# Performance work log

Hardware: AMD Instinct MI355X
Metric: run time of the kernel (lower is better)

Reference implementation:

```python
import jax, jax.numpy as jnp
import numpy as np

B, S = 8, 512          # batch, seq_len
D, F = 1024, 2048      # d_model, head hidden dim
H = 16                 # num_tasks (= num heads)
V = 3000               # selfies vocab
O = 1                  # head output size
INIT = 0.02


def setup_inputs() -> dict:
    key = jax.random.key(0)
    ks = jax.random.split(key, 12)
    return {
        "selfies": jax.random.randint(ks[0], (B, S), 0, V),
        "tasks": jax.random.randint(ks[1], (B, S), 0, H + 1),  # 0 -> invalid (-1)
        "values": jax.random.normal(ks[2], (B, S), jnp.float32),
        "property_mask": jax.random.randint(ks[3], (B, S), 0, 2).astype(bool),
        # shared_base params (embed + FFN -> [B,S,D])
        "emb_selfies": jax.random.normal(ks[4], (V, D), jnp.float32) * INIT,
        "emb_tasks": jax.random.normal(ks[5], (H + 1, D), jnp.float32) * INIT,
        "val_vec": jax.random.normal(ks[6], (D,), jnp.float32) * INIT,
        "Ws": jax.random.normal(ks[7], (D, D), jnp.float32) * INIT,
        "bs": jnp.zeros((D,), jnp.float32),
        # stacked per-head MLP params: Linear(D,F) -> GELU -> Linear(F,O)
        "W1": jax.random.normal(ks[8], (H, D, F), jnp.float32) * INIT,
        "b1": jnp.zeros((H, F), jnp.float32),
        "W2": jax.random.normal(ks[9], (H, F, O), jnp.float32) * INIT,
        "b2": jnp.zeros((H, O), jnp.float32),
    }


def reference(selfies, tasks, values, property_mask,
              emb_selfies, emb_tasks, val_vec, Ws, bs, W1, b1, W2, b2):
    # ---- shared_base: embed + masked token features + FFN -> [B,S,D] ----
    h = (emb_selfies[selfies] + emb_tasks[tasks] + values[..., None] * val_vec)
    h = h * property_mask[..., None].astype(h.dtype)
    shared = jax.nn.gelu(h @ Ws + bs)                      # [B,S,D]

    # ---- routing: task token -> head index, 0 means invalid (-1) ----
    head_idx = jnp.where(tasks > 0, (tasks - 1) % H, -1)   # [B,S]

    # ---- each active head runs its MLP over the FULL shared_output ----
    hid = jax.nn.gelu(jnp.einsum('bsd,hdf->bshf', shared, W1) + b1)  # [B,S,H,F]
    heads_out = jnp.einsum('bshf,hfo->bsho', hid, W2) + b2           # [B,S,H,O]

    # ---- scatter/select per token by head index; invalid -> zeros ----
    idx = jnp.clip(head_idx, 0)
    out = jnp.take_along_axis(heads_out, idx[..., None, None], axis=2)[:, :, 0, :]
    return jnp.where(head_idx[..., None] >= 0, out, jnp.zeros_like(out))
```

## Files before the change

### kernel.cpp

```cpp
#include <hip/hip_runtime.h>
#include <hip/hip_bf16.h>

#define TOK 4096
#define DD  1024
#define FF  2048
#define NH  16

typedef short bf16x8 __attribute__((ext_vector_type(8)));
typedef float f32x4  __attribute__((ext_vector_type(4)));

__device__ __forceinline__ float gelu_f(float x) {
  float u = 0.7978845608028654f * (x + 0.044715f * x * x * x);
  float e = __expf(2.0f * u);
  return 0.5f * x * (2.0f - 2.0f / (e + 1.0f));
}

__device__ __forceinline__ unsigned short f2bf(float f) {
  union { float f; unsigned u; } v; v.f = f;
  unsigned r = v.u + 0x7FFF + ((v.u >> 16) & 1);
  return (unsigned short)(r >> 16);
}
__device__ __forceinline__ unsigned pack2(float a, float b) {
  return (unsigned)f2bf(a) | ((unsigned)f2bf(b) << 16);
}

__device__ __forceinline__ void load_lds16(const void* g, void* l) {
  __builtin_amdgcn_global_load_lds(
      (const __attribute__((address_space(1))) void*)g,
      (__attribute__((address_space(3))) void*)l, 16, 0, 0);
}

__global__ __launch_bounds__(256) void route_kernel(
    const int* __restrict__ tasks, const float* __restrict__ b2,
    int* __restrict__ counts, int* __restrict__ lists, float* __restrict__ out) {
  int t = blockIdx.x * 256 + threadIdx.x;
  if (t >= TOK) return;
  int task = tasks[t];
  if (task > 0) {
    int h = (task - 1) & (NH - 1);
    int pos = atomicAdd(&counts[h], 1);
    lists[h * TOK + pos] = t;
    out[t] = b2[h];
  } else {
    out[t] = 0.0f;
  }
}

__global__ __launch_bounds__(256) void prep_x(
    const int* __restrict__ selfies, const int* __restrict__ tasks,
    const float* __restrict__ values, const int* __restrict__ pmask,
    const float* __restrict__ emb_s, const float* __restrict__ emb_t,
    const float* __restrict__ val_vec, unsigned short* __restrict__ Xb) {
  int gid = blockIdx.x * 256 + threadIdx.x;
  int kc = (gid & 127) * 8;
  int t  = gid >> 7;
  int sid = selfies[t], tsk = tasks[t];
  float v = values[t];
  float msk = pmask[t] ? 1.0f : 0.0f;
  const float* ps = emb_s + (size_t)sid * DD + kc;
  const float* pt = emb_t + (size_t)tsk * DD + kc;
  const float* pv = val_vec + kc;
  float r[8];
#pragma unroll
  for (int j = 0; j < 8; j += 4) {
    float4 a = *(const float4*)(ps + j);
    float4 b = *(const float4*)(pt + j);
    float4 c = *(const float4*)(pv + j);
    r[j + 0] = (a.x + b.x + v * c.x) * msk;
    r[j + 1] = (a.y + b.y + v * c.y) * msk;
    r[j + 2] = (a.z + b.z + v * c.z) * msk;
    r[j + 3] = (a.w + b.w + v * c.w) * msk;
  }
  uint4 o;
  o.x = pack2(r[0], r[1]); o.y = pack2(r[2], r[3]);
  o.z = pack2(r[4], r[5]); o.w = pack2(r[6], r[7]);
  *(uint4*)(Xb + (size_t)gid * 8) = o;
}

__global__ __launch_bounds__(256) void prep_w(
    const float* __restrict__ Ws, const float* __restrict__ W1,
    unsigned short* __restrict__ Wsp, unsigned short* __restrict__ W1p) {
  int cid = blockIdx.x * 256 + threadIdx.x;
  const float* src;
  unsigned short* dst;
  int stride;
  if (cid < 16 * 128 * 32 * 64) {
    int lane = cid & 63, kc2 = (cid >> 6) & 31, nt = (cid >> 11) & 127, h = cid >> 18;
    src = W1 + ((size_t)h * DD + kc2 * 32 + (lane >> 4) * 8) * FF + nt * 16 + (lane & 15);
    dst = W1p + (size_t)cid * 8;
    stride = FF;
  } else {
    int cid2 = cid - 16 * 128 * 32 * 64;
    int lane = cid2 & 63, kc2 = (cid2 >> 6) & 31, nt = cid2 >> 11;
    src = Ws + ((size_t)kc2 * 32 + (lane >> 4) * 8) * DD + nt * 16 + (lane & 15);
    dst = Wsp + (size_t)cid2 * 8;
    stride = DD;
  }
  float r[8];
#pragma unroll
  for (int j = 0; j < 8; ++j) r[j] = src[(size_t)j * stride];
  uint4 o;
  o.x = pack2(r[0], r[1]); o.y = pack2(r[2], r[3]);
  o.z = pack2(r[4], r[5]); o.w = pack2(r[6], r[7]);
  *(uint4*)dst = o;
}

__global__ __launch_bounds__(256) void gemm1_mfma(
    const unsigned short* __restrict__ Xb, const unsigned short* __restrict__ Wsp,
    const float* __restrict__ bs, unsigned short* __restrict__ shared_bf) {
  __shared__ __align__(16) unsigned short As[2 * 4 * 64 * 8];
  __shared__ __align__(16) unsigned short Bs[2 * 8 * 64 * 8];

  const int tid = threadIdx.x;
  const int lane = tid & 63, w = tid >> 6;
  const int m0 = blockIdx.x * 64;
  const int n0 = blockIdx.y * 128;
  const int q = lane >> 4, c = lane & 15;

  const unsigned short* aSrc = Xb + (size_t)(m0 + w * 16 + c) * DD + q * 8;
  unsigned short* aDst0 = As + (size_t)(0 * 256 + w * 64 + lane) * 8;
  unsigned short* aDst1 = As + (size_t)(1 * 256 + w * 64 + lane) * 8;

  const unsigned short* bBase = Wsp + ((size_t)(blockIdx.y * 8 + w * 2)) * 32 * 512 + lane * 8;
  f32x4 acc[4][2] = {};

  for (int k0 = 0; k0 < DD; k0 += 64) {
    load_lds16(aSrc + k0, aDst0);
    load_lds16(aSrc + k0 + 32, aDst1);
    const unsigned short* bk = bBase + k0 * 16;
#pragma unroll
    for (int i = 0; i < 4; ++i) {
      int kk = i >> 1, t = i & 1;
      load_lds16(bk + (size_t)t * 16384 + kk * 512,
                 Bs + (size_t)(kk * 8 + w * 2 + t) * 512 + lane * 8);
    }
    __syncthreads();
#pragma unroll
    for (int kk = 0; kk < 2; ++kk) {
      bf16x8 a[4], b[2];
#pragma unroll
      for (int mt = 0; mt < 4; ++mt)
        a[mt] = *(const bf16x8*)(As + (size_t)((kk * 4 + mt) * 64 + lane) * 8);
#pragma unroll
      for (int t = 0; t < 2; ++t)
        b[t] = *(const bf16x8*)(Bs + (size_t)((kk * 8 + w * 2 + t) * 64 + lane) * 8);
#pragma unroll
      for (int mt = 0; mt < 4; ++mt)
#pragma unroll
        for (int t = 0; t < 2; ++t)
          acc[mt][t] = __builtin_amdgcn_mfma_f32_16x16x32_bf16(a[mt], b[t], acc[mt][t], 0, 0, 0);
    }
    __syncthreads();
  }

  float bsv[2];
#pragma unroll
  for (int t = 0; t < 2; ++t) bsv[t] = bs[n0 + w * 32 + t * 16 + c];
#pragma unroll
  for (int mt = 0; mt < 4; ++mt)
#pragma unroll
    for (int t = 0; t < 2; ++t)
#pragma unroll
      for (int r = 0; r < 4; ++r) {
        int row = m0 + mt * 16 + q * 4 + r;
        int col = n0 + w * 32 + t * 16 + c;
        shared_bf[(size_t)row * DD + col] = f2bf(gelu_f(acc[mt][t][r] + bsv[t]));
      }
}

__global__ __launch_bounds__(256) void gemm2_mfma(
    const unsigned short* __restrict__ shared_bf, const unsigned short* __restrict__ W1p,
    const float* __restrict__ b1, const float* __restrict__ W2,
    const int* __restrict__ counts, const int* __restrict__ lists,
    float* __restrict__ out) {
  const int h = blockIdx.z;
  const int nt_h = counts[h];
  const int m0 = blockIdx.x * 64;
  if (m0 >= nt_h) return;
  const int fc = blockIdx.y;

  __shared__ __align__(16) unsigned short As[2 * 4 * 64 * 8];
  __shared__ __align__(16) unsigned short Bs[2 * 16 * 64 * 8];
  __shared__ int   stok[64];
  __shared__ float red[4][68];

  const int tid = threadIdx.x;
  const int lane = tid & 63, w = tid >> 6;
  const int q = lane >> 4, c = lane & 15;

  if (tid < 64) {
    int i = m0 + tid;
    stok[tid] = (i < nt_h) ? lists[h * TOK + i] : -1;
  }
  __syncthreads();

  int tokr = stok[w * 16 + c];
  if (tokr < 0) tokr = 0;
  const unsigned short* aSrc = shared_bf + (size_t)tokr * DD + q * 8;
  unsigned short* aDst0 = As + (size_t)(0 * 256 + w * 64 + lane) * 8;
  unsigned short* aDst1 = As + (size_t)(1 * 256 + w * 64 + lane) * 8;

  const unsigned short* bBase =
      W1p + ((size_t)h * 128 + fc * 16 + w * 4) * 32 * 512 + lane * 8;

  f32x4 acc[4][4] = {};

  for (int k0 = 0; k0 < DD; k0 += 64) {
    load_lds16(aSrc + k0, aDst0);
    load_lds16(aSrc + k0 + 32, aDst1);
    const unsigned short* bk = bBase + k0 * 16;
#pragma unroll
    for (int i = 0; i < 8; ++i) {
      int kk = i >> 2, t = i & 3;
      load_lds16(bk + (size_t)t * 16384 + kk * 512,
                 Bs + (size_t)(kk * 16 + w * 4 + t) * 512 + lane * 8);
    }
    __syncthreads();
#pragma unroll
    for (int kk = 0; kk < 2; ++kk) {
      bf16x8 a[4], b[4];
#pragma unroll
      for (int mt = 0; mt < 4; ++mt)
        a[mt] = *(const bf16x8*)(As + (size_t)((kk * 4 + mt) * 64 + lane) * 8);
#pragma unroll
      for (int t = 0; t < 4; ++t)
        b[t] = *(const bf16x8*)(Bs + (size_t)((kk * 16 + w * 4 + t) * 64 + lane) * 8);
#pragma unroll
      for (int mt = 0; mt < 4; ++mt)
#pragma unroll
        for (int t = 0; t < 4; ++t)
          acc[mt][t] = __builtin_amdgcn_mfma_f32_16x16x32_bf16(a[mt], b[t], acc[mt][t], 0, 0, 0);
    }
    __syncthreads();
  }

  const float* b1h = b1 + (size_t)h * FF + fc * 256 + w * 64;
  const float* w2h = W2 + (size_t)h * FF + fc * 256 + w * 64;
  float b1v[4], w2v[4];
#pragma unroll
  for (int t = 0; t < 4; ++t) { b1v[t] = b1h[t * 16 + c]; w2v[t] = w2h[t * 16 + c]; }

#pragma unroll
  for (int mt = 0; mt < 4; ++mt)
#pragma unroll
    for (int r = 0; r < 4; ++r) {
      float s = 0.0f;
#pragma unroll
      for (int t = 0; t < 4; ++t)
        s += gelu_f(acc[mt][t][r] + b1v[t]) * w2v[t];
      s += __shfl_xor(s, 1);
      s += __shfl_xor(s, 2);
      s += __shfl_xor(s, 4);
      s += __shfl_xor(s, 8);
      if (c == 0) red[w][mt * 16 + q * 4 + r] = s;
    }
  __syncthreads();

  if (tid < 64) {
    int t = stok[tid];
    if (t >= 0) {
      float s = red[0][tid] + red[1][tid] + red[2][tid] + red[3][tid];
      atomicAdd(&out[t], s);
    }
  }
}

extern "C" void kernel_launch(void* const* d_in, const int* in_sizes, int n_in,
                              void* d_out, int out_size, void* d_ws, size_t ws_size,
                              hipStream_t stream) {
  const int*   selfies = (const int*)d_in[0];
  const int*   tasks   = (const int*)d_in[1];
  const float* values  = (const float*)d_in[2];
  const int*   pmask   = (const int*)d_in[3];
  const float* emb_s   = (const float*)d_in[4];
  const float* emb_t   = (const float*)d_in[5];
  const float* val_vec = (const float*)d_in[6];
  const float* Ws      = (const float*)d_in[7];
  const float* bs      = (const float*)d_in[8];
  const float* W1      = (const float*)d_in[9];
  const float* b1      = (const float*)d_in[10];
  const float* W2      = (const float*)d_in[11];
  const float* b2      = (const float*)d_in[12];
  float* out = (float*)d_out;

  char* ws = (char*)d_ws;
  unsigned short* Xb        = (unsigned short*)ws;
  unsigned short* shared_bf = (unsigned short*)(ws + (8u << 20));
  unsigned short* Wsp       = (unsigned short*)(ws + (16u << 20));
  unsigned short* W1p       = (unsigned short*)(ws + (18u << 20));
  int* counts = (int*)(ws + (82u << 20));
  int* lists  = (int*)(ws + (82u << 20) + 256);

  hipMemsetAsync(counts, 0, NH * sizeof(int), stream);
  route_kernel<<<TOK / 256, 256, 0, stream>>>(tasks, b2, counts, lists, out);
  prep_x<<<TOK * 128 / 256, 256, 0, stream>>>(selfies, tasks, values, pmask,
                                              emb_s, emb_t, val_vec, Xb);
  prep_w<<<(16 * 128 * 32 * 64 + 64 * 32 * 64) / 256, 256, 0, stream>>>(Ws, W1, Wsp, W1p);
  gemm1_mfma<<<dim3(TOK / 64, DD / 128), 256, 0, stream>>>(Xb, Wsp, bs, shared_bf);
  gemm2_mfma<<<dim3(8, FF / 256, NH), 256, 0, stream>>>(shared_bf, W1p, b1, W2,
                                                        counts, lists, out);
}
```

Baseline: 353.0 us.

## Double-buffer LDS in both GEMMs and halve gemm2 N-tile width

Both MFMA GEMM kernels now keep two LDS buffers, so the next k-slice is loaded while the current one is computed, with one barrier per iteration instead of two. gemm2 also narrows its F tile from 256 to 128 columns per block and doubles the grid along F, which lowers accumulator register use and adds more blocks. The cost is reloading the A tile twice as often in gemm2 and using more LDS per block.

Result: no change. 358.8 us (+1.6%).

```diff
diff --git a/kernel.cpp b/kernel.cpp
--- a/kernel.cpp
+++ b/kernel.cpp
@@ -108,8 +108,8 @@
 __global__ __launch_bounds__(256) void gemm1_mfma(
     const unsigned short* __restrict__ Xb, const unsigned short* __restrict__ Wsp,
     const float* __restrict__ bs, unsigned short* __restrict__ shared_bf) {
-  __shared__ __align__(16) unsigned short As[2 * 4 * 64 * 8];
-  __shared__ __align__(16) unsigned short Bs[2 * 8 * 64 * 8];
+  __shared__ __align__(16) unsigned short As[2][2 * 4 * 64 * 8];
+  __shared__ __align__(16) unsigned short Bs[2][2 * 8 * 64 * 8];
 
   const int tid = threadIdx.x;
   const int lane = tid & 63, w = tid >> 6;
@@ -118,40 +118,48 @@
   const int q = lane >> 4, c = lane & 15;
 
   const unsigned short* aSrc = Xb + (size_t)(m0 + w * 16 + c) * DD + q * 8;
-  unsigned short* aDst0 = As + (size_t)(0 * 256 + w * 64 + lane) * 8;
-  unsigned short* aDst1 = As + (size_t)(1 * 256 + w * 64 + lane) * 8;
-
   const unsigned short* bBase = Wsp + ((size_t)(blockIdx.y * 8 + w * 2)) * 32 * 512 + lane * 8;
   f32x4 acc[4][2] = {};
 
-  for (int k0 = 0; k0 < DD; k0 += 64) {
-    load_lds16(aSrc + k0, aDst0);
-    load_lds16(aSrc + k0 + 32, aDst1);
+  auto stage = [&](int buf, int k0) {
+    load_lds16(aSrc + k0,      As[buf] + (size_t)(0 * 256 + w * 64 + lane) * 8);
+    load_lds16(aSrc + k0 + 32, As[buf] + (size_t)(1 * 256 + w * 64 + lane) * 8);
     const unsigned short* bk = bBase + k0 * 16;
 #pragma unroll
     for (int i = 0; i < 4; ++i) {
       int kk = i >> 1, t = i & 1;
       load_lds16(bk + (size_t)t * 16384 + kk * 512,
-                 Bs + (size_t)(kk * 8 + w * 2 + t) * 512 + lane * 8);
-    }
-    __syncthreads();
+                 Bs[buf] + (size_t)(kk * 8 + w * 2 + t) * 512 + lane * 8);
+    }
+  };
+  auto compute = [&](int buf) {
 #pragma unroll
     for (int kk = 0; kk < 2; ++kk) {
       bf16x8 a[4], b[2];
 #pragma unroll
       for (int mt = 0; mt < 4; ++mt)
-        a[mt] = *(const bf16x8*)(As + (size_t)((kk * 4 + mt) * 64 + lane) * 8);
+        a[mt] = *(const bf16x8*)(As[buf] + (size_t)((kk * 4 + mt) * 64 + lane) * 8);
 #pragma unroll
       for (int t = 0; t < 2; ++t)
-        b[t] = *(const bf16x8*)(Bs + (size_t)((kk * 8 + w * 2 + t) * 64 + lane) * 8);
+        b[t] = *(const bf16x8*)(Bs[buf] + (size_t)((kk * 8 + w * 2 + t) * 64 + lane) * 8);
 #pragma unroll
       for (int mt = 0; mt < 4; ++mt)
 #pragma unroll
         for (int t = 0; t < 2; ++t)
           acc[mt][t] = __builtin_amdgcn_mfma_f32_16x16x32_bf16(a[mt], b[t], acc[mt][t], 0, 0, 0);
     }
+  };
+
+  stage(0, 0);
+  __syncthreads();
+  int cur = 0;
+  for (int k0 = 64; k0 < DD; k0 += 64) {
+    stage(cur ^ 1, k0);
+    compute(cur);
     __syncthreads();
-  }
+    cur ^= 1;
+  }
+  compute(cur);
 
   float bsv[2];
 #pragma unroll
@@ -179,8 +187,8 @@
   if (m0 >= nt_h) return;
   const int fc = blockIdx.y;
 
-  __shared__ __align__(16) unsigned short As[2 * 4 * 64 * 8];
-  __shared__ __align__(16) unsigned short Bs[2 * 16 * 64 * 8];
+  __shared__ __align__(16) unsigned short As[2][2 * 4 * 64 * 8];
+  __shared__ __align__(16) unsigned short Bs[2][2 * 8 * 64 * 8];
   __shared__ int   stok[64];
   __shared__ float red[4][68];
 
@@ -197,48 +205,57 @@
   int tokr = stok[w * 16 + c];
   if (tokr < 0) tokr = 0;
   const unsigned short* aSrc = shared_bf + (size_t)tokr * DD + q * 8;
-  unsigned short* aDst0 = As + (size_t)(0 * 256 + w * 64 + lane) * 8;
-  unsigned short* aDst1 = As + (size_t)(1 * 256 + w * 64 + lane) * 8;
 
   const unsigned short* bBase =
-      W1p + ((size_t)h * 128 + fc * 16 + w * 4) * 32 * 512 + lane * 8;
-
-  f32x4 acc[4][4] = {};
-
-  for (int k0 = 0; k0 < DD; k0 += 64) {
-    load_lds16(aSrc + k0, aDst0);
-    load_lds16(aSrc + k0 + 32, aDst1);
+      W1p + ((size_t)h * 128 + fc * 8 + w * 2) * 32 * 512 + lane * 8;
+
+  f32x4 acc[4][2] = {};
+
+  auto stage = [&](int buf, int k0) {
+    load_lds16(aSrc + k0,      As[buf] + (size_t)(0 * 256 + w * 64 + lane) * 8);
+    load_lds16(aSrc + k0 + 32, As[buf] + (size_t)(1 * 256 + w * 64 + lane) * 8);
     const unsigned short* bk = bBase + k0 * 16;
 #pragma unroll
-    for (int i = 0; i < 8; ++i) {
-      int kk = i >> 2, t = i & 3;
+    for (int i = 0; i < 4; ++i) {
+      int kk = i >> 1, t = i & 1;
       load_lds16(bk + (size_t)t * 16384 + kk * 512,
-                 Bs + (size_t)(kk * 16 + w * 4 + t) * 512 + lane * 8);
-    }
+                 Bs[buf] + (size_t)(kk * 8 + w * 2 + t) * 512 + lane * 8);
+    }
+  };
+  auto compute = [&](int buf) {
+#pragma unroll
+    for (int kk = 0; kk < 2; ++kk) {
+      bf16x8 a[4], b[2];
+#pragma unroll
+      for (int mt = 0; mt < 4; ++mt)
+        a[mt] = *(const bf16x8*)(As[buf] + (size_t)((kk * 4 + mt) * 64 + lane) * 8);
+#pragma unroll
+      for (int t = 0; t < 2; ++t)
+        b[t] = *(const bf16x8*)(Bs[buf] + (size_t)((kk * 8 + w * 2 + t) * 64 + lane) * 8);
+#pragma unroll
+      for (int mt = 0; mt < 4; ++mt)
+#pragma unroll
+        for (int t = 0; t < 2; ++t)
+          acc[mt][t] = __builtin_amdgcn_mfma_f32_16x16x32_bf16(a[mt], b[t], acc[mt][t], 0, 0, 0);
+    }
+  };
+
+  stage(0, 0);
+  __syncthreads();
+  int cur = 0;
+  for (int k0 = 64; k0 < DD; k0 += 64) {
+    stage(cur ^ 1, k0);
+    compute(cur);
     __syncthreads();
-#pragma unroll
-    for (int kk = 0; kk < 2; ++kk) {
-      bf16x8 a[4], b[4];
-#pragma unroll
-      for (int mt = 0; mt < 4; ++mt)
-        a[mt] = *(const bf16x8*)(As + (size_t)((kk * 4 + mt) * 64 + lane) * 8);
-#pragma unroll
-      for (int t = 0; t < 4; ++t)
-        b[t] = *(const bf16x8*)(Bs + (size_t)((kk * 16 + w * 4 + t) * 64 + lane) * 8);
-#pragma unroll
-      for (int mt = 0; mt < 4; ++mt)
-#pragma unroll
-        for (int t = 0; t < 4; ++t)
-          acc[mt][t] = __builtin_amdgcn_mfma_f32_16x16x32_bf16(a[mt], b[t], acc[mt][t], 0, 0, 0);
-    }
-    __syncthreads();
-  }
-
-  const float* b1h = b1 + (size_t)h * FF + fc * 256 + w * 64;
-  const float* w2h = W2 + (size_t)h * FF + fc * 256 + w * 64;
-  float b1v[4], w2v[4];
-#pragma unroll
-  for (int t = 0; t < 4; ++t) { b1v[t] = b1h[t * 16 + c]; w2v[t] = w2h[t * 16 + c]; }
+    cur ^= 1;
+  }
+  compute(cur);
+
+  const float* b1h = b1 + (size_t)h * FF + fc * 128 + w * 32;
+  const float* w2h = W2 + (size_t)h * FF + fc * 128 + w * 32;
+  float b1v[2], w2v[2];
+#pragma unroll
+  for (int t = 0; t < 2; ++t) { b1v[t] = b1h[t * 16 + c]; w2v[t] = w2h[t * 16 + c]; }
 
 #pragma unroll
   for (int mt = 0; mt < 4; ++mt)
@@ -246,7 +263,7 @@
     for (int r = 0; r < 4; ++r) {
       float s = 0.0f;
 #pragma unroll
-      for (int t = 0; t < 4; ++t)
+      for (int t = 0; t < 2; ++t)
         s += gelu_f(acc[mt][t][r] + b1v[t]) * w2v[t];
       s += __shfl_xor(s, 1);
       s += __shfl_xor(s, 2);
@@ -297,6 +314,6 @@
                                               emb_s, emb_t, val_vec, Xb);
   prep_w<<<(16 * 128 * 32 * 64 + 64 * 32 * 64) / 256, 256, 0, stream>>>(Ws, W1, Wsp, W1p);
   gemm1_mfma<<<dim3(TOK / 64, DD / 128), 256, 0, stream>>>(Xb, Wsp, bs, shared_bf);
-  gemm2_mfma<<<dim3(8, FF / 256, NH), 256, 0, stream>>>(shared_bf, W1p, b1, W2,
+  gemm2_mfma<<<dim3(8, FF / 128, NH), 256, 0, stream>>>(shared_bf, W1p, b1, W2,
                                                         counts, lists, out);
 }
```
